# Optimization experiments

Measured on AMD Instinct MI355X. Metric: run time of the kernel, lower is better.

The kernel has to match this reference:

```python
import jax, jax.numpy as jnp
import numpy as np

K = 3  # sparsify_graph default k


def _lstm_dir(x, Wi, Wh, b, reverse):
    # x: [B, T, Hin]; Wi: [Hin, 4H]; Wh: [H, 4H]; b: [4H]
    B = x.shape[0]
    H = Wh.shape[0]
    xs = jnp.swapaxes(x, 0, 1)  # [T, B, Hin]
    if reverse:
        xs = xs[::-1]

    def step(carry, xt):
        h, c = carry
        g = xt @ Wi + h @ Wh + b
        i, f, gg, o = jnp.split(g, 4, axis=-1)  # torch gate order i,f,g,o
        c = jax.nn.sigmoid(f) * c + jax.nn.sigmoid(i) * jnp.tanh(gg)
        h = jax.nn.sigmoid(o) * jnp.tanh(c)
        return (h, c), h

    h0 = jnp.zeros((B, H), x.dtype)
    _, hs = jax.lax.scan(step, (h0, h0), xs)
    if reverse:
        hs = hs[::-1]
    return jnp.swapaxes(hs, 0, 1)  # [B, T, H]


def setup_inputs() -> dict:
    key = jax.random.key(0)
    ks = jax.random.split(key, 24)
    B, T, C, F = 16, 256, 64, 128
    GO, H = 32, 32  # gat_out, lstm hidden
    s = 0.1
    return {
        "x": jax.random.normal(ks[0], (B, T, C, F), jnp.float32),
        "spectral_w": jax.random.normal(ks[1], (C, F), jnp.float32),
        "gat_W": jax.random.normal(ks[2], (F, GO), jnp.float32) * s,
        "gat_a": jax.random.normal(ks[3], (2 * GO,), jnp.float32),
        "pool_w": jax.random.normal(ks[4], (GO, 1), jnp.float32) * s,
        "pool_b": jnp.zeros((1,), jnp.float32),
        "lstm_Wi_f": jax.random.normal(ks[5], (GO, 4 * H), jnp.float32) * s,
        "lstm_Wh_f": jax.random.normal(ks[6], (H, 4 * H), jnp.float32) * s,
        "lstm_b_f": jnp.zeros((4 * H,), jnp.float32),
        "lstm_Wi_r": jax.random.normal(ks[7], (GO, 4 * H), jnp.float32) * s,
        "lstm_Wh_r": jax.random.normal(ks[8], (H, 4 * H), jnp.float32) * s,
        "lstm_b_r": jnp.zeros((4 * H,), jnp.float32),
        "ta_W": jax.random.normal(ks[9], (2 * H, 2 * H), jnp.float32) * s,
        "ta_b": jnp.zeros((2 * H,), jnp.float32),
        "ta_v": jax.random.normal(ks[10], (2 * H,), jnp.float32) * s,
        "ln_g": jnp.ones((2 * H,), jnp.float32),
        "ln_b": jnp.zeros((2 * H,), jnp.float32),
        "fc1_w": jax.random.normal(ks[11], (2 * H, 32), jnp.float32) * s,
        "fc1_b": jnp.zeros((32,), jnp.float32),
        "fc2_w": jax.random.normal(ks[12], (32, 3), jnp.float32) * s,
        "fc2_b": jnp.zeros((3,), jnp.float32),
    }


def reference(x, spectral_w, gat_W, gat_a, pool_w, pool_b,
              lstm_Wi_f, lstm_Wh_f, lstm_b_f, lstm_Wi_r, lstm_Wh_r, lstm_b_r,
              ta_W, ta_b, ta_v, ln_g, ln_b, fc1_w, fc1_b, fc2_w, fc2_b):
    B, T, C, F = x.shape
    # SpectralWeighting: per-(channel,feature) softmaxed weights over feature dim
    x = x * jax.nn.softmax(spectral_w, axis=-1)  # [B,T,C,F]

    # compute_graph per sample: mean_t of cosine-similarity Gram over channels
    Hn = x / (jnp.linalg.norm(x, axis=-1, keepdims=True) + 1e-8)
    A = jnp.einsum('btcf,btdf->bcd', Hn, Hn) / T  # [B,C,C]

    # sparsify_graph: per-row top-(K+1), drop diagonal, symmetrize mask
    _, idx = jax.lax.top_k(A, K + 1)  # [B,C,K+1]
    topk_mask = jnp.sum(jax.nn.one_hot(idx, C, dtype=jnp.float32), axis=2) > 0  # [B,C,C]
    eye = jnp.eye(C, dtype=bool)
    topk_mask = topk_mask & ~eye
    topk_mask = topk_mask | jnp.swapaxes(topk_mask, 1, 2)
    A = jnp.where(topk_mask, A, 0.0)

    # GAT layer, vectorized over (B, T) with shared per-sample adjacency
    Wh = jnp.einsum('btcf,fo->btco', x, gat_W)  # [B,T,C,32]
    O = Wh.shape[-1]
    s1 = Wh @ gat_a[:O]  # [B,T,C]  a . Wh_i
    s2 = Wh @ gat_a[O:]  # [B,T,C]  a . Wh_j
    e = jax.nn.leaky_relu(s1[..., :, None] + s2[..., None, :], 0.2)  # [B,T,C,C]
    amask = (A > 0) | eye  # [B,C,C]
    e = jnp.where(amask[:, None], e, -1e9)
    alpha = jax.nn.softmax(e, axis=-1)  # dropout skipped (eval mode)
    gat = jax.nn.relu(jnp.einsum('btcd,btdo->btco', alpha, Wh))  # [B,T,C,32]

    # ChannelAttentionPooling: softmax over channel dim
    w = jax.nn.softmax(gat @ pool_w + pool_b, axis=2)  # [B,T,C,1]
    h = jnp.sum(gat * w, axis=2)  # [B,T,32]

    # BiLSTM
    hf = _lstm_dir(h, lstm_Wi_f, lstm_Wh_f, lstm_b_f, False)
    hr = _lstm_dir(h, lstm_Wi_r, lstm_Wh_r, lstm_b_r, True)
    h = jnp.concatenate([hf, hr], axis=-1)  # [B,T,64]

    # TemporalAttention (dropout skipped, eval mode)
    sc = (jnp.tanh(h @ ta_W + ta_b) @ ta_v) / 1.5  # [B,T]
    al = jax.nn.softmax(sc, axis=1)
    ctx = jnp.sum(h * al[..., None], axis=1)  # [B,64]

    # LayerNorm
    mu = jnp.mean(ctx, axis=-1, keepdims=True)
    var = jnp.var(ctx, axis=-1, keepdims=True)
    ctx = (ctx - mu) / jnp.sqrt(var + 1e-5) * ln_g + ln_b

    # Classifier head (dropout skipped, eval mode)
    return jax.nn.relu(ctx @ fc1_w + fc1_b) @ fc2_w + fc2_b  # [B,3]
```

## Files before the change

kernel.cpp:

```cpp
#include <hip/hip_runtime.h>
#include <hip/hip_bf16.h>

#define B_  16
#define T_  256
#define C_  64
#define F_  128
#define O_  32
#define H_  32
#define G4_ 128

typedef __attribute__((ext_vector_type(8))) short bfrag;
typedef __attribute__((ext_vector_type(4))) float f4acc;

__device__ __forceinline__ unsigned short f2bf(float v) {
    union { float f; unsigned u; } c; c.f = v;
    unsigned r = c.u + 0x7FFF + ((c.u >> 16) & 1);
    return (unsigned short)(r >> 16);
}
__device__ __forceinline__ float bf2f(unsigned short b) {
    union { float f; unsigned u; } c; c.u = ((unsigned)b) << 16; return c.f;
}
__device__ __forceinline__ float sigm_f(float x) {
    return __builtin_amdgcn_rcpf(1.f + __expf(-x));
}
__device__ __forceinline__ float tanh_f(float x) {
    float e = __expf(2.f * x);
    return 1.f - 2.f * __builtin_amdgcn_rcpf(e + 1.f);
}
__device__ __forceinline__ float readlane_f(float v, int l) {
    return __int_as_float(__builtin_amdgcn_readlane(__float_as_int(v), l));
}

__global__ __launch_bounds__(64) void k_sw(const float* __restrict__ w,
                                           float* __restrict__ sw) {
    int c = blockIdx.x, lane = threadIdx.x;
    const float* row = w + c * F_;
    float v0 = row[lane], v1 = row[lane + 64];
    float m = fmaxf(v0, v1);
#pragma unroll
    for (int s = 1; s < 64; s <<= 1) m = fmaxf(m, __shfl_xor(m, s));
    float e0 = __expf(v0 - m), e1 = __expf(v1 - m);
    float s = e0 + e1;
#pragma unroll
    for (int s_ = 1; s_ < 64; s_ <<= 1) s += __shfl_xor(s, s_);
    sw[c * F_ + lane] = e0 / s;
    sw[c * F_ + lane + 64] = e1 / s;
}

#define TCP 2
#define PSTR 136

#define MFMA16(a, b, c) __builtin_amdgcn_mfma_f32_16x16x32_bf16(a, b, c, 0, 0, 0)

__global__ __launch_bounds__(256) void k_phase1(
    const float* __restrict__ x, const float* __restrict__ sw,
    const float* __restrict__ gat_W, const float* __restrict__ gat_a,
    float* __restrict__ A, float* __restrict__ Wh,
    float* __restrict__ s1, float* __restrict__ s2) {
    const int b = blockIdx.x, tc = blockIdx.y, tid = threadIdx.x;
    const int wv = tid >> 6, lane = tid & 63;
    const int quad = lane >> 4, l16 = lane & 15;

    __shared__ unsigned short hhi[64 * PSTR];
    __shared__ unsigned short hlo[64 * PSTR];
    __shared__ float nrm[64];
    __shared__ float s1p[2][64], s2p[2][64];

    float4 swr[8];
    {
        const float4* sw4 = (const float4*)sw;
#pragma unroll
        for (int i = 0; i < 8; i++) swr[i] = sw4[tid + 256 * i];
    }

    const int rt0 = (wv >> 1) * 2;
    const int ct0 = (wv & 1) * 2;
    const int jW = wv & 1;

    bfrag wfh[4], wfl[4];
    {
        const int n = l16 + 16 * jW;
#pragma unroll
        for (int k = 0; k < 4; k++) {
            union { unsigned short u[8]; bfrag v; } Hu, Lu;
#pragma unroll
            for (int u = 0; u < 8; u++) {
                float v = gat_W[(32 * k + quad * 8 + u) * O_ + n];
                unsigned short hb = f2bf(v);
                Hu.u[u] = hb;
                Lu.u[u] = f2bf(v - bf2f(hb));
            }
            wfh[k] = Hu.v;
            wfl[k] = Lu.v;
        }
    }
    const float ga1 = gat_a[l16 + 16 * jW];
    const float ga2 = gat_a[O_ + l16 + 16 * jW];

    f4acc accA[2][2];
#pragma unroll
    for (int i = 0; i < 2; i++)
#pragma unroll
        for (int j = 0; j < 2; j++) accA[i][j] = (f4acc){0.f, 0.f, 0.f, 0.f};

    for (int tt = 0; tt < TCP; ++tt) {
        const int t = tc * TCP + tt;
        const float4* xg = (const float4*)(x + ((size_t)(b * T_ + t) << 13));
        float4 xr[8];
#pragma unroll
        for (int i = 0; i < 8; i++) xr[i] = xg[tid + 256 * i];

        float invn_[8];
#pragma unroll
        for (int i = 0; i < 8; i++) {
            float4 v = xr[i], s = swr[i];
            v.x *= s.x; v.y *= s.y; v.z *= s.z; v.w *= s.w;
            xr[i] = v;
            float ss = v.x * v.x + v.y * v.y + v.z * v.z + v.w * v.w;
#pragma unroll
            for (int d = 1; d < 32; d <<= 1) ss += __shfl_xor(ss, d);
            float nv = sqrtf(ss) + 1e-8f;
            invn_[i] = 1.0f / nv;
            if ((tid & 31) == 0) nrm[(tid >> 5) + 8 * i] = nv;
        }
#pragma unroll
        for (int i = 0; i < 8; i++) {
            int c = (tid >> 5) + 8 * i;
            float4 v = xr[i];
            float iv = invn_[i];
            float a0 = v.x * iv, a1 = v.y * iv, a2 = v.z * iv, a3 = v.w * iv;
            union { unsigned short u[4]; unsigned long long q; } Hq, Lq;
            unsigned short h0 = f2bf(a0), h1 = f2bf(a1), h2 = f2bf(a2), h3 = f2bf(a3);
            Hq.u[0] = h0; Hq.u[1] = h1; Hq.u[2] = h2; Hq.u[3] = h3;
            Lq.u[0] = f2bf(a0 - bf2f(h0));
            Lq.u[1] = f2bf(a1 - bf2f(h1));
            Lq.u[2] = f2bf(a2 - bf2f(h2));
            Lq.u[3] = f2bf(a3 - bf2f(h3));
            int off = c * PSTR + 4 * (tid & 31);
            *(unsigned long long*)&hhi[off] = Hq.q;
            *(unsigned long long*)&hlo[off] = Lq.q;
        }
        __syncthreads();

        f4acc accW0 = (f4acc){0.f, 0.f, 0.f, 0.f};
        f4acc accW1 = (f4acc){0.f, 0.f, 0.f, 0.f};
#pragma unroll
        for (int k = 0; k < 4; k++) {
            const int ko = 32 * k + 8 * quad;
            bfrag r0h = *(const bfrag*)&hhi[(rt0 * 16 + l16) * PSTR + ko];
            bfrag r0l = *(const bfrag*)&hlo[(rt0 * 16 + l16) * PSTR + ko];
            bfrag r1h = *(const bfrag*)&hhi[((rt0 + 1) * 16 + l16) * PSTR + ko];
            bfrag r1l = *(const bfrag*)&hlo[((rt0 + 1) * 16 + l16) * PSTR + ko];
            bfrag c0h = *(const bfrag*)&hhi[(ct0 * 16 + l16) * PSTR + ko];
            bfrag c0l = *(const bfrag*)&hlo[(ct0 * 16 + l16) * PSTR + ko];
            bfrag c1h = *(const bfrag*)&hhi[((ct0 + 1) * 16 + l16) * PSTR + ko];
            bfrag c1l = *(const bfrag*)&hlo[((ct0 + 1) * 16 + l16) * PSTR + ko];
            accA[0][0] = MFMA16(r0h, c0h, accA[0][0]);
            accA[0][0] = MFMA16(r0h, c0l, accA[0][0]);
            accA[0][0] = MFMA16(r0l, c0h, accA[0][0]);
            accA[0][1] = MFMA16(r0h, c1h, accA[0][1]);
            accA[0][1] = MFMA16(r0h, c1l, accA[0][1]);
            accA[0][1] = MFMA16(r0l, c1h, accA[0][1]);
            accA[1][0] = MFMA16(r1h, c0h, accA[1][0]);
            accA[1][0] = MFMA16(r1h, c0l, accA[1][0]);
            accA[1][0] = MFMA16(r1l, c0h, accA[1][0]);
            accA[1][1] = MFMA16(r1h, c1h, accA[1][1]);
            accA[1][1] = MFMA16(r1h, c1l, accA[1][1]);
            accA[1][1] = MFMA16(r1l, c1h, accA[1][1]);
            accW0 = MFMA16(r0h, wfh[k], accW0);
            accW0 = MFMA16(r0h, wfl[k], accW0);
            accW0 = MFMA16(r0l, wfh[k], accW0);
            accW1 = MFMA16(r1h, wfh[k], accW1);
            accW1 = MFMA16(r1h, wfl[k], accW1);
            accW1 = MFMA16(r1l, wfh[k], accW1);
        }
        float* whout = Wh + (size_t)(b * T_ + t) * (C_ * O_);
#pragma unroll
        for (int i2 = 0; i2 < 2; i2++) {
            f4acc aw = i2 ? accW1 : accW0;
#pragma unroll
            for (int r = 0; r < 4; r++) {
                int row = (rt0 + i2) * 16 + quad * 4 + r;
                float val = aw[r] * nrm[row];
                whout[row * O_ + l16 + 16 * jW] = val;
                float v1 = val * ga1, v2 = val * ga2;
#pragma unroll
                for (int d = 1; d < 16; d <<= 1) {
                    v1 += __shfl_xor(v1, d);
                    v2 += __shfl_xor(v2, d);
                }
                if (l16 == 0) { s1p[jW][row] = v1; s2p[jW][row] = v2; }
            }
        }
        __syncthreads();
        if (tid < 64) {
            s1[(b * T_ + t) * C_ + tid] = s1p[0][tid] + s1p[1][tid];
            s2[(b * T_ + t) * C_ + tid] = s2p[0][tid] + s2p[1][tid];
        }
    }
#pragma unroll
    for (int i2 = 0; i2 < 2; i2++)
#pragma unroll
        for (int j2 = 0; j2 < 2; j2++)
#pragma unroll
            for (int r = 0; r < 4; r++) {
                int row = (rt0 + i2) * 16 + quad * 4 + r;
                int col = (ct0 + j2) * 16 + l16;
                atomicAdd(&A[b * (C_ * C_) + row * C_ + col], accA[i2][j2][r]);
            }
}

__global__ __launch_bounds__(64) void k_topk(const float* __restrict__ A,
                                             unsigned long long* __restrict__ amask) {
    int b = blockIdx.x;
    int c = threadIdx.x;
    __shared__ unsigned long long tk[C_];
    const float* row = A + b * (C_ * C_) + c * C_;
    unsigned long long sel = 0ULL;
    for (int r = 0; r < 4; r++) {
        float best = -1e30f;
        int bi = 0;
        for (int d = 0; d < C_; d++) {
            if (sel & (1ULL << d)) continue;
            float v = row[d];
            if (v > best) { best = v; bi = d; }
        }
        sel |= (1ULL << bi);
    }
    unsigned long long t = sel & ~(1ULL << c);
    tk[c] = t;
    __syncthreads();
    unsigned long long sym = t;
    for (int d = 0; d < C_; d++)
        if ((tk[d] >> c) & 1ULL) sym |= (1ULL << d);
    unsigned long long m = (1ULL << c);
    unsigned long long s2 = sym;
    while (s2) {
        int d = __ffsll(s2) - 1;
        s2 &= s2 - 1;
        if (row[d] > 0.f) m |= (1ULL << d);
    }
    amask[b * C_ + c] = m;
}

__global__ __launch_bounds__(256) void k_gat(
    const float* __restrict__ Wh, const float* __restrict__ s1,
    const float* __restrict__ s2, const unsigned long long* __restrict__ amask,
    const float* __restrict__ pool_w, const float* __restrict__ pool_b,
    const float* __restrict__ Wi_f, const float* __restrict__ b_f,
    const float* __restrict__ Wi_r, const float* __restrict__ b_r,
    float* __restrict__ gx) {
    int tg = blockIdx.x;
    int wv = threadIdx.x >> 6, c = threadIdx.x & 63;
    int bt = tg * 4 + wv;
    int b = bt >> 8;
    __shared__ float buf[4][C_][33];
    __shared__ float s2s[4][C_];
    __shared__ float hp[4][H_];

    s2s[wv][c] = s2[bt * C_ + c];
    float s1c = s1[bt * C_ + c];
    unsigned long long m = amask[b * C_ + c];
    __syncthreads();

    float mx = -1e30f;
    unsigned long long mm = m;
    while (mm) {
        int d = __ffsll(mm) - 1; mm &= mm - 1;
        float v = s1c + s2s[wv][d];
        v = v > 0.f ? v : 0.2f * v;
        mx = fmaxf(mx, v);
    }
    float ssum = 0.f;
    mm = m;
    while (mm) {
        int d = __ffsll(mm) - 1; mm &= mm - 1;
        float v = s1c + s2s[wv][d];
        v = v > 0.f ? v : 0.2f * v;
        ssum += __expf(v - mx);
    }
    float inv = 1.0f / ssum;
    float g[O_];
#pragma unroll
    for (int i = 0; i < O_; i++) g[i] = 0.f;
    mm = m;
    while (mm) {
        int d = __ffsll(mm) - 1; mm &= mm - 1;
        float v = s1c + s2s[wv][d];
        v = v > 0.f ? v : 0.2f * v;
        float a = __expf(v - mx);
        const float4* wr = (const float4*)(Wh + (size_t)bt * (C_ * O_) + d * O_);
#pragma unroll
        for (int q = 0; q < 8; q++) {
            float4 w4 = wr[q];
            g[4 * q + 0] += a * w4.x;
            g[4 * q + 1] += a * w4.y;
            g[4 * q + 2] += a * w4.z;
            g[4 * q + 3] += a * w4.w;
        }
    }
    float lg = pool_b[0];
#pragma unroll
    for (int i = 0; i < O_; i++) {
        g[i] = fmaxf(g[i] * inv, 0.f);
        lg += g[i] * pool_w[i];
    }
    float wmx = lg;
#pragma unroll
    for (int s = 1; s < 64; s <<= 1) wmx = fmaxf(wmx, __shfl_xor(wmx, s));
    float we = __expf(lg - wmx);
    float wsum = we;
#pragma unroll
    for (int s = 1; s < 64; s <<= 1) wsum += __shfl_xor(wsum, s);
    float wcf = we / wsum;
#pragma unroll
    for (int i = 0; i < O_; i++) buf[wv][c][i] = g[i] * wcf;
    __syncthreads();
    {
        int wt = threadIdx.x >> 6, o = threadIdx.x & 31, hf = (threadIdx.x >> 5) & 1;
        float sacc = 0.f;
#pragma unroll 8
        for (int d = hf * 32; d < hf * 32 + 32; d++) sacc += buf[wt][d][o];
        sacc += __shfl_xor(sacc, 32);
        if (hf == 0) hp[wt][o] = sacc;
    }
    __syncthreads();
    {
        int dir = threadIdx.x >> 7, col = threadIdx.x & 127;
        const float* Wi = dir ? Wi_r : Wi_f;
        const float* bb = dir ? b_r : b_f;
        float bv = bb[col];
        float a0 = bv, a1 = bv, a2 = bv, a3 = bv;
#pragma unroll
        for (int k = 0; k < H_; k++) {
            float wvv = Wi[k * G4_ + col];
            a0 = fmaf(hp[0][k], wvv, a0);
            a1 = fmaf(hp[1][k], wvv, a1);
            a2 = fmaf(hp[2][k], wvv, a2);
            a3 = fmaf(hp[3][k], wvv, a3);
        }
        int b0 = (tg * 4) >> 8;
        int t0 = (tg * 4) & 255;
        float* cb = gx + ((size_t)(dir * B_ + b0) * G4_ + col) * T_;
        if (dir == 0) {
            *(float4*)(cb + t0) = make_float4(a0, a1, a2, a3);
        } else {
            *(float4*)(cb + (252 - t0)) = make_float4(a3, a2, a1, a0);
        }
    }
}

#define WW(k) float2 ww##k = make_float2(Wd[(k) * G4_ + lane], Wd[(k) * G4_ + lane + 64]);
#define KST(k, Aq) { float hk = readlane_f(h, k); \
    Aq.x = fmaf(hk, ww##k.x, Aq.x); Aq.y = fmaf(hk, ww##k.y, Aq.y); }

#define STEP(G0, G1) { \
    float2 A0 = make_float2(G0, G1); \
    float2 A1 = make_float2(0.f, 0.f); \
    float2 A2 = make_float2(0.f, 0.f); \
    float2 A3 = make_float2(0.f, 0.f); \
    KST(0, A0)  KST(1, A1)  KST(2, A2)  KST(3, A3) \
    KST(4, A0)  KST(5, A1)  KST(6, A2)  KST(7, A3) \
    KST(8, A0)  KST(9, A1)  KST(10, A2) KST(11, A3) \
    KST(12, A0) KST(13, A1) KST(14, A2) KST(15, A3) \
    KST(16, A0) KST(17, A1) KST(18, A2) KST(19, A3) \
    KST(20, A0) KST(21, A1) KST(22, A2) KST(23, A3) \
    KST(24, A0) KST(25, A1) KST(26, A2) KST(27, A3) \
    KST(28, A0) KST(29, A1) KST(30, A2) KST(31, A3) \
    float g0 = (A0.x + A1.x) + (A2.x + A3.x); \
    float g1 = (A0.y + A1.y) + (A2.y + A3.y); \
    float sA = sigm_f(g0); \
    float u = sigm_f(half_sel * g1); \
    float sB = (lane < 32) ? fmaf(2.f, u, -1.f) : u; \
    float sf = __shfl(sA, (lane & 31) + 32); \
    float so = __shfl(sB, (lane & 31) + 32); \
    cst = fmaf(sf, cst, sA * sB); \
    float hn = so * tanh_f(cst); \
    h = hn; \
    if (lane < H_) *hc = hn; \
    hc += hstride; \
}

__global__ void __attribute__((amdgpu_flat_work_group_size(64, 64)))
__attribute__((amdgpu_waves_per_eu(1, 1))) k_lstm_seq(
    const float* __restrict__ gx,
    const float* __restrict__ Whf, const float* __restrict__ Whr,
    float* __restrict__ hcat) {
    int dir = blockIdx.x & 1, b = blockIdx.x >> 1;
    int lane = threadIdx.x;
    const float* Wd = dir ? Whr : Whf;
    WW(0) WW(1) WW(2) WW(3) WW(4) WW(5) WW(6) WW(7)
    WW(8) WW(9) WW(10) WW(11) WW(12) WW(13) WW(14) WW(15)
    WW(16) WW(17) WW(18) WW(19) WW(20) WW(21) WW(22) WW(23)
    WW(24) WW(25) WW(26) WW(27) WW(28) WW(29) WW(30) WW(31)

    const float* p0 = gx + ((size_t)(dir * B_ + b) * G4_ + lane) * T_;
    const float* p1 = p0 + (size_t)64 * T_;
    float* hc = hcat + ((size_t)(b * T_) + (dir ? T_ - 1 : 0)) * (2 * H_)
                + dir * H_ + lane;
    const int hstride = dir ? -(2 * H_) : (2 * H_);

    float h = 0.f, cst = 0.f;
    const float half_sel = (lane < 32) ? 2.f : 1.f;

    float4 c0a = *(const float4*)(p0 + 0);
    float4 c0b = *(const float4*)(p0 + 4);
    float4 c1a = *(const float4*)(p1 + 0);
    float4 c1b = *(const float4*)(p1 + 4);

    for (int bi = 0; bi < 32; bi++) {
        int o = (8 * (bi + 1)) & 255;
        float4 n0a = *(const float4*)(p0 + o);
        float4 n0b = *(const float4*)(p0 + o + 4);
        float4 n1a = *(const float4*)(p1 + o);
        float4 n1b = *(const float4*)(p1 + o + 4);

        STEP(c0a.x, c1a.x)
        STEP(c0a.y, c1a.y)
        STEP(c0a.z, c1a.z)
        STEP(c0a.w, c1a.w)
        STEP(c0b.x, c1b.x)
        STEP(c0b.y, c1b.y)
        STEP(c0b.z, c1b.z)
        STEP(c0b.w, c1b.w)

        c0a = n0a; c0b = n0b; c1a = n1a; c1b = n1b;
    }
}

__global__ __launch_bounds__(256) void k_final(
    const float* __restrict__ hcat,
    const float* __restrict__ taW, const float* __restrict__ tab,
    const float* __restrict__ tav,
    const float* __restrict__ lng, const float* __restrict__ lnb,
    const float* __restrict__ w1, const float* __restrict__ b1,
    const float* __restrict__ w2, const float* __restrict__ b2,
    float* __restrict__ out) {
    int b = blockIdx.x;
    int t = threadIdx.x;
    __shared__ float Wl[64 * 64];
    __shared__ float al[T_];
    __shared__ float wred[4];
    __shared__ float ctxp[4][64];
    __shared__ float ctx[64];
    __shared__ float a1[32];
    for (int i = t; i < 4096; i += 256) Wl[i] = taW[i];
    float4 hr[16];
    const float4* hb = (const float4*)(hcat + ((size_t)b * T_ + t) * 64);
#pragma unroll
    for (int i = 0; i < 16; i++) hr[i] = hb[i];
    __syncthreads();
    float sc = 0.f;
    for (int j = 0; j < 64; j++) {
        float s = tab[j];
#pragma unroll
        for (int k4 = 0; k4 < 16; k4++) {
            float4 h4 = hr[k4];
            const float* wcol = &Wl[(4 * k4) * 64 + j];
            s += h4.x * wcol[0] + h4.y * wcol[64] + h4.z * wcol[128] + h4.w * wcol[192];
        }
        sc += tanhf(s) * tav[j];
    }
    sc *= (1.0f / 1.5f);
    int wave = t >> 6, lane = t & 63;
    float m = sc;
#pragma unroll
    for (int s_ = 1; s_ < 64; s_ <<= 1) m = fmaxf(m, __shfl_xor(m, s_));
    if (lane == 0) wred[wave] = m;
    __syncthreads();
    m = fmaxf(fmaxf(wred[0], wred[1]), fmaxf(wred[2], wred[3]));
    float e = __expf(sc - m);
    float ssum = e;
#pragma unroll
    for (int s_ = 1; s_ < 64; s_ <<= 1) ssum += __shfl_xor(ssum, s_);
    __syncthreads();
    if (lane == 0) wred[wave] = ssum;
    __syncthreads();
    float S = wred[0] + wred[1] + wred[2] + wred[3];
    al[t] = e / S;
    __syncthreads();
    {
        int o = t & 63, part = t >> 6;
        float cacc = 0.f;
        for (int tt = part * 64; tt < part * 64 + 64; tt++)
            cacc += al[tt] * hcat[((size_t)b * T_ + tt) * 64 + o];
        ctxp[part][o] = cacc;
    }
    __syncthreads();
    if (t < 64) {
        float ctxo = ctxp[0][t] + ctxp[1][t] + ctxp[2][t] + ctxp[3][t];
        float sv = ctxo, sq = ctxo * ctxo;
#pragma unroll
        for (int s_ = 1; s_ < 64; s_ <<= 1) {
            sv += __shfl_xor(sv, s_);
            sq += __shfl_xor(sq, s_);
        }
        float mu = sv * (1.f / 64.f);
        float var = sq * (1.f / 64.f) - mu * mu;
        ctx[t] = (ctxo - mu) / sqrtf(var + 1e-5f) * lng[t] + lnb[t];
    }
    __syncthreads();
    if (t < 32) {
        float s = b1[t];
        for (int k = 0; k < 64; k++) s += ctx[k] * w1[k * 32 + t];
        a1[t] = fmaxf(s, 0.f);
    }
    __syncthreads();
    if (t < 3) {
        float s = b2[t];
        for (int k = 0; k < 32; k++) s += a1[k] * w2[k * 3 + t];
        out[b * 3 + t] = s;
    }
}

extern "C" void kernel_launch(void* const* d_in, const int* in_sizes, int n_in,
                              void* d_out, int out_size, void* d_ws, size_t ws_size,
                              hipStream_t stream) {
    const float* x          = (const float*)d_in[0];
    const float* spectral_w = (const float*)d_in[1];
    const float* gat_W      = (const float*)d_in[2];
    const float* gat_a      = (const float*)d_in[3];
    const float* pool_w     = (const float*)d_in[4];
    const float* pool_b     = (const float*)d_in[5];
    const float* lstm_Wi_f  = (const float*)d_in[6];
    const float* lstm_Wh_f  = (const float*)d_in[7];
    const float* lstm_b_f   = (const float*)d_in[8];
    const float* lstm_Wi_r  = (const float*)d_in[9];
    const float* lstm_Wh_r  = (const float*)d_in[10];
    const float* lstm_b_r   = (const float*)d_in[11];
    const float* ta_W       = (const float*)d_in[12];
    const float* ta_b       = (const float*)d_in[13];
    const float* ta_v       = (const float*)d_in[14];
    const float* ln_g       = (const float*)d_in[15];
    const float* ln_b       = (const float*)d_in[16];
    const float* fc1_w      = (const float*)d_in[17];
    const float* fc1_b      = (const float*)d_in[18];
    const float* fc2_w      = (const float*)d_in[19];
    const float* fc2_b      = (const float*)d_in[20];
    float* out = (float*)d_out;

    float* ws = (float*)d_ws;
    float* sw    = ws + 0;
    float* A     = ws + 8192;
    unsigned long long* amask = (unsigned long long*)(ws + 73728);
    float* Wh    = ws + 75776;
    float* s1    = ws + 8464384;
    float* s2    = ws + 8726528;
    float* gx    = ws + 9119744;
    float* hcat  = ws + 10168320;

    hipMemsetAsync(A, 0, (size_t)C_ * C_ * B_ * sizeof(float), stream);
    k_sw<<<C_, 64, 0, stream>>>(spectral_w, sw);
    k_phase1<<<dim3(B_, T_ / TCP), 256, 0, stream>>>(x, sw, gat_W, gat_a, A, Wh, s1, s2);
    k_topk<<<B_, 64, 0, stream>>>(A, amask);
    k_gat<<<B_ * T_ / 4, 256, 0, stream>>>(Wh, s1, s2, amask, pool_w, pool_b,
                                           lstm_Wi_f, lstm_b_f, lstm_Wi_r, lstm_b_r, gx);
    k_lstm_seq<<<2 * B_, 64, 0, stream>>>(gx, lstm_Wh_f, lstm_Wh_r, hcat);
    k_final<<<B_, 256, 0, stream>>>(hcat, ta_W, ta_b, ta_v, ln_g, ln_b,
                                    fc1_w, fc1_b, fc2_w, fc2_b, out);
}
```

Before: 454.5 us.

## Pack forward and reverse LSTM directions into one wave per batch

The recurrent LSTM kernel now runs both directions in one 64-lane wave per batch element. Lanes 0-31 handle forward and lanes 32-63 reverse, and each lane owns one hidden unit and computes all four gates with 128 register-held weights. The hidden-state broadcast now uses a shuffle within each half instead of readlane. This halves the block count and removes the cross-lane gate exchange, but each step issues four times as many FMAs per lane and carries much more register pressure on the serial critical path.

```diff
diff --git a/kernel.cpp b/kernel.cpp
--- a/kernel.cpp
+++ b/kernel.cpp
@@ -26,9 +26,6 @@
 __device__ __forceinline__ float tanh_f(float x) {
     float e = __expf(2.f * x);
     return 1.f - 2.f * __builtin_amdgcn_rcpf(e + 1.f);
-}
-__device__ __forceinline__ float readlane_f(float v, int l) {
-    return __int_as_float(__builtin_amdgcn_readlane(__float_as_int(v), l));
 }
 
 __global__ __launch_bounds__(64) void k_sw(const float* __restrict__ w,
@@ -350,35 +347,24 @@
     }
 }
 
-#define WW(k) float2 ww##k = make_float2(Wd[(k) * G4_ + lane], Wd[(k) * G4_ + lane + 64]);
-#define KST(k, Aq) { float hk = readlane_f(h, k); \
-    Aq.x = fmaf(hk, ww##k.x, Aq.x); Aq.y = fmaf(hk, ww##k.y, Aq.y); }
-
-#define STEP(G0, G1) { \
-    float2 A0 = make_float2(G0, G1); \
-    float2 A1 = make_float2(0.f, 0.f); \
-    float2 A2 = make_float2(0.f, 0.f); \
-    float2 A3 = make_float2(0.f, 0.f); \
-    KST(0, A0)  KST(1, A1)  KST(2, A2)  KST(3, A3) \
-    KST(4, A0)  KST(5, A1)  KST(6, A2)  KST(7, A3) \
-    KST(8, A0)  KST(9, A1)  KST(10, A2) KST(11, A3) \
-    KST(12, A0) KST(13, A1) KST(14, A2) KST(15, A3) \
-    KST(16, A0) KST(17, A1) KST(18, A2) KST(19, A3) \
-    KST(20, A0) KST(21, A1) KST(22, A2) KST(23, A3) \
-    KST(24, A0) KST(25, A1) KST(26, A2) KST(27, A3) \
-    KST(28, A0) KST(29, A1) KST(30, A2) KST(31, A3) \
-    float g0 = (A0.x + A1.x) + (A2.x + A3.x); \
-    float g1 = (A0.y + A1.y) + (A2.y + A3.y); \
-    float sA = sigm_f(g0); \
-    float u = sigm_f(half_sel * g1); \
-    float sB = (lane < 32) ? fmaf(2.f, u, -1.f) : u; \
-    float sf = __shfl(sA, (lane & 31) + 32); \
-    float so = __shfl(sB, (lane & 31) + 32); \
-    cst = fmaf(sf, cst, sA * sB); \
-    float hn = so * tanh_f(cst); \
+#define KS(k) { float hk = __shfl(h, brd + k); \
+    ai = fmaf(hk, wi[k], ai); af = fmaf(hk, wf[k], af); \
+    ag = fmaf(hk, wg[k], ag); ao = fmaf(hk, wo[k], ao); }
+
+#define STEPL(GI, GF, GG, GO) { \
+    float ai = GI, af = GF, ag = GG, ao = GO; \
+    KS(0)  KS(1)  KS(2)  KS(3)  KS(4)  KS(5)  KS(6)  KS(7) \
+    KS(8)  KS(9)  KS(10) KS(11) KS(12) KS(13) KS(14) KS(15) \
+    KS(16) KS(17) KS(18) KS(19) KS(20) KS(21) KS(22) KS(23) \
+    KS(24) KS(25) KS(26) KS(27) KS(28) KS(29) KS(30) KS(31) \
+    float sI = sigm_f(ai); \
+    float sF = sigm_f(af); \
+    float sG = tanh_f(ag); \
+    float sO = sigm_f(ao); \
+    cst = fmaf(sF, cst, sI * sG); \
+    float hn = sO * tanh_f(cst); \
     h = hn; \
-    if (lane < H_) *hc = hn; \
-    hc += hstride; \
+    *hc = hn; hc += hstride; \
 }
 
 __global__ void __attribute__((amdgpu_flat_work_group_size(64, 64)))
@@ -386,45 +372,57 @@
     const float* __restrict__ gx,
     const float* __restrict__ Whf, const float* __restrict__ Whr,
     float* __restrict__ hcat) {
-    int dir = blockIdx.x & 1, b = blockIdx.x >> 1;
+    int b = blockIdx.x;
     int lane = threadIdx.x;
-    const float* Wd = dir ? Whr : Whf;
-    WW(0) WW(1) WW(2) WW(3) WW(4) WW(5) WW(6) WW(7)
-    WW(8) WW(9) WW(10) WW(11) WW(12) WW(13) WW(14) WW(15)
-    WW(16) WW(17) WW(18) WW(19) WW(20) WW(21) WW(22) WW(23)
-    WW(24) WW(25) WW(26) WW(27) WW(28) WW(29) WW(30) WW(31)
-
-    const float* p0 = gx + ((size_t)(dir * B_ + b) * G4_ + lane) * T_;
-    const float* p1 = p0 + (size_t)64 * T_;
-    float* hc = hcat + ((size_t)(b * T_) + (dir ? T_ - 1 : 0)) * (2 * H_)
-                + dir * H_ + lane;
-    const int hstride = dir ? -(2 * H_) : (2 * H_);
+    int j = lane & 31;
+    const int brd = lane & 32;
+    const float* Wsel = (lane < 32) ? Whf : Whr;
+
+    float wi[32], wf[32], wg[32], wo[32];
+#pragma unroll
+    for (int k = 0; k < 32; k++) {
+        wi[k] = Wsel[k * G4_ + j];
+        wf[k] = Wsel[k * G4_ + 32 + j];
+        wg[k] = Wsel[k * G4_ + 64 + j];
+        wo[k] = Wsel[k * G4_ + 96 + j];
+    }
+
+    const int dblk = (lane < 32) ? b : (B_ + b);
+    const float* pi = gx + ((size_t)dblk * G4_ + 0  + j) * T_;
+    const float* pf = gx + ((size_t)dblk * G4_ + 32 + j) * T_;
+    const float* pg = gx + ((size_t)dblk * G4_ + 64 + j) * T_;
+    const float* po = gx + ((size_t)dblk * G4_ + 96 + j) * T_;
+
+    float* hc = (lane < 32)
+        ? (hcat + (size_t)(b * T_) * 64 + j)
+        : (hcat + ((size_t)(b * T_) + T_ - 1) * 64 + 32 + j);
+    const int hstride = (lane < 32) ? 64 : -64;
 
     float h = 0.f, cst = 0.f;
-    const float half_sel = (lane < 32) ? 2.f : 1.f;
-
-    float4 c0a = *(const float4*)(p0 + 0);
-    float4 c0b = *(const float4*)(p0 + 4);
-    float4 c1a = *(const float4*)(p1 + 0);
-    float4 c1b = *(const float4*)(p1 + 4);
+
+    float4 ia = *(const float4*)(pi + 0), ib = *(const float4*)(pi + 4);
+    float4 fa = *(const float4*)(pf + 0), fb = *(const float4*)(pf + 4);
+    float4 ga = *(const float4*)(pg + 0), gb = *(const float4*)(pg + 4);
+    float4 oa = *(const float4*)(po + 0), ob = *(const float4*)(po + 4);
 
     for (int bi = 0; bi < 32; bi++) {
         int o = (8 * (bi + 1)) & 255;
-        float4 n0a = *(const float4*)(p0 + o);
-        float4 n0b = *(const float4*)(p0 + o + 4);
-        float4 n1a = *(const float4*)(p1 + o);
-        float4 n1b = *(const float4*)(p1 + o + 4);
-
-        STEP(c0a.x, c1a.x)
-        STEP(c0a.y, c1a.y)
-        STEP(c0a.z, c1a.z)
-        STEP(c0a.w, c1a.w)
-        STEP(c0b.x, c1b.x)
-        STEP(c0b.y, c1b.y)
-        STEP(c0b.z, c1b.z)
-        STEP(c0b.w, c1b.w)
-
-        c0a = n0a; c0b = n0b; c1a = n1a; c1b = n1b;
+        float4 nia = *(const float4*)(pi + o), nib = *(const float4*)(pi + o + 4);
+        float4 nfa = *(const float4*)(pf + o), nfb = *(const float4*)(pf + o + 4);
+        float4 nga = *(const float4*)(pg + o), ngb = *(const float4*)(pg + o + 4);
+        float4 noa = *(const float4*)(po + o), nob = *(const float4*)(po + o + 4);
+
+        STEPL(ia.x, fa.x, ga.x, oa.x)
+        STEPL(ia.y, fa.y, ga.y, oa.y)
+        STEPL(ia.z, fa.z, ga.z, oa.z)
+        STEPL(ia.w, fa.w, ga.w, oa.w)
+        STEPL(ib.x, fb.x, gb.x, ob.x)
+        STEPL(ib.y, fb.y, gb.y, ob.y)
+        STEPL(ib.z, fb.z, gb.z, ob.z)
+        STEPL(ib.w, fb.w, gb.w, ob.w)
+
+        ia = nia; ib = nib; fa = nfa; fb = nfb;
+        ga = nga; gb = ngb; oa = noa; ob = nob;
     }
 }
 
@@ -555,7 +553,7 @@
     k_topk<<<B_, 64, 0, stream>>>(A, amask);
     k_gat<<<B_ * T_ / 4, 256, 0, stream>>>(Wh, s1, s2, amask, pool_w, pool_b,
                                            lstm_Wi_f, lstm_b_f, lstm_Wi_r, lstm_b_r, gx);
-    k_lstm_seq<<<2 * B_, 64, 0, stream>>>(gx, lstm_Wh_f, lstm_Wh_r, hcat);
+    k_lstm_seq<<<B_, 64, 0, stream>>>(gx, lstm_Wh_f, lstm_Wh_r, hcat);
     k_final<<<B_, 256, 0, stream>>>(hcat, ta_W, ta_b, ta_v, ln_g, ln_b,
                                     fc1_w, fc1_b, fc2_w, fc2_b, out);
 }
```

After: 522.2 us. 14.9% more time.
